# Kernel optimization log

Hardware: AMD Instinct MI355X
Metric: run time of the kernel (lower is better)

## Reference

```python
import jax, jax.numpy as jnp
import numpy as np

B, C, CE, DK, DV, H, W = 2, 64, 96, 64, 64, 96, 96
EPS = 1e-6


def setup_inputs() -> dict:
    key = jax.random.key(0)
    ks = jax.random.split(key, 8)
    s = lambda fan_in: 1.0 / np.sqrt(fan_in)
    return {
        "x": jax.random.normal(ks[0], (B, C, H, W), jnp.float32),
        "x_enc": jax.random.normal(ks[1], (B, CE, H, W), jnp.float32),
        "Wq": jax.random.uniform(ks[2], (DK, CE), jnp.float32, -s(CE), s(CE)),
        "bq": jax.random.uniform(ks[3], (DK,), jnp.float32, -s(CE), s(CE)),
        "Wk": jax.random.uniform(ks[4], (DK, CE), jnp.float32, -s(CE), s(CE)),
        "bk": jax.random.uniform(ks[5], (DK,), jnp.float32, -s(CE), s(CE)),
        "Wv": jax.random.uniform(ks[6], (DV, C), jnp.float32, -s(C), s(C)),
        "bv": jax.random.uniform(ks[7], (DV,), jnp.float32, -s(C), s(C)),
    }


def _l2norm(t):
    # F.normalize(dim=1): divide by channel-dim L2 norm, clamped at eps
    n = jnp.maximum(jnp.linalg.norm(t, axis=1, keepdims=True), EPS)
    return t / n


def reference(x, x_enc, Wq, bq, Wk, bk, Wv, bv):
    # 1x1 conv projections == pointwise channel GEMMs
    Q = jnp.einsum('oc,bchw->bohw', Wq, x_enc) + bq[None, :, None, None]
    K = jnp.einsum('oc,bchw->bohw', Wk, x_enc) + bk[None, :, None, None]
    V = jnp.einsum('oc,bchw->bohw', Wv, x) + bv[None, :, None, None]
    vshape = V.shape
    Q = _l2norm(Q.reshape(B, DK, H * W))  # [B, dk, L]
    K = _l2norm(K.reshape(B, DK, H * W))
    V = V.reshape(B, DV, H * W)           # [B, dv, L]
    # cosine-similarity attention over all spatial positions: A is [B, L, L]
    A = jax.nn.softmax(jnp.einsum('bqi,bqj->bij', Q, K), axis=-1)
    R = jnp.einsum('bij,bvj->bvi', A, V)   # [B, dv, L]
    return R.reshape(vshape)
```

## Files before the change

kernel.cpp:

```cpp
#include <hip/hip_runtime.h>

#define L_ 9216
#define TPS 9

typedef unsigned int uint;
typedef unsigned short ushort;
typedef __attribute__((ext_vector_type(8))) short short8;
typedef __attribute__((ext_vector_type(4))) float f32x4;
typedef __attribute__((ext_vector_type(16))) float f32x16;
typedef __attribute__((ext_vector_type(4))) unsigned uint4v;
typedef __attribute__((ext_vector_type(2))) unsigned uint2v;

#define MFMA32(a, b, c) __builtin_amdgcn_mfma_f32_32x32x16_bf16(a, b, c, 0, 0, 0)

#if __has_builtin(__builtin_amdgcn_exp2f)
#define EXP2(x) __builtin_amdgcn_exp2f(x)
#else
#define EXP2(x) exp2f(x)
#endif

#define GLOAD_LDS16(g, l)                                            \
  __builtin_amdgcn_global_load_lds(                                  \
      (const __attribute__((address_space(1))) unsigned int*)(g),    \
      (__attribute__((address_space(3))) unsigned int*)(l), 16, 0, 0)

union B8 {
  uint4v u;
  short8 s;
};

__device__ __forceinline__ ushort f2bf(float f) {
  uint u = __float_as_uint(f);
  return (ushort)((u + 0x7fffu + ((u >> 16) & 1u)) >> 16);
}

__device__ __forceinline__ f32x16 zero16() {
  f32x16 v;
#pragma unroll
  for (int i = 0; i < 16; i++) v[i] = 0.f;
  return v;
}

__global__ __launch_bounds__(256) void prep_kernel(
    const float* __restrict__ Wq, const float* __restrict__ Wk,
    const float* __restrict__ Wv, ushort* __restrict__ Wqb,
    ushort* __restrict__ Wkb, ushort* __restrict__ Wvb) {
  int i = blockIdx.x * 256 + threadIdx.x;
  if (i < 6144) {
    Wqb[i] = f2bf(Wq[i]);
    Wkb[i] = f2bf(Wk[i]);
  }
  if (i < 4096) Wvb[i] = f2bf(Wv[i]);
}

template <int CC, int TASK>
__device__ __forceinline__ void projm_body(
    const float* __restrict__ X,
    const ushort* __restrict__ Wb,
    const float* __restrict__ bias,
    ushort* __restrict__ dst) {
  constexpr int NKT = CC / 16;
  const int bx = blockIdx.x;
  const int b = bx / 288;
  const int p0 = (bx - b * 288) * 32;
  const int lane = threadIdx.x;
  const int ql = lane & 31;
  const int hs = lane >> 5;

  const float* Xb = X + (size_t)b * CC * L_ + p0 + ql;
  float xv[NKT * 8];
#pragma unroll
  for (int kt = 0; kt < NKT; kt++)
#pragma unroll
    for (int i = 0; i < 8; i++)
      xv[kt * 8 + i] = Xb[(size_t)(kt * 16 + hs * 8 + i) * L_];

  B8 bfr[NKT];
#pragma unroll
  for (int kt = 0; kt < NKT; kt++)
#pragma unroll
    for (int j = 0; j < 4; j++) {
      uint lo = f2bf(xv[kt * 8 + 2 * j]);
      uint hi = f2bf(xv[kt * 8 + 2 * j + 1]);
      bfr[kt].u[j] = lo | (hi << 16);
    }

  const ushort* Wr0 = Wb + (size_t)ql * CC + hs * 8;
  const ushort* Wr1 = Wb + (size_t)(32 + ql) * CC + hs * 8;

  f32x16 a0 = zero16(), a1 = zero16();
#pragma unroll
  for (int kt = 0; kt < NKT; kt++) {
    short8 w0 = *(const short8*)(Wr0 + kt * 16);
    short8 w1 = *(const short8*)(Wr1 + kt * 16);
    a0 = MFMA32(w0, bfr[kt].s, a0);
    a1 = MFMA32(w1, bfr[kt].s, a1);
  }

#pragma unroll
  for (int g = 0; g < 4; g++) {
    float4 b0 = *(const float4*)(bias + 8 * g + 4 * hs);
    float4 b1 = *(const float4*)(bias + 32 + 8 * g + 4 * hs);
    a0[4 * g + 0] += b0.x; a0[4 * g + 1] += b0.y;
    a0[4 * g + 2] += b0.z; a0[4 * g + 3] += b0.w;
    a1[4 * g + 0] += b1.x; a1[4 * g + 1] += b1.y;
    a1[4 * g + 2] += b1.z; a1[4 * g + 3] += b1.w;
  }

  if (TASK < 2) {
    float ss = 0.f;
#pragma unroll
    for (int r = 0; r < 16; r++) ss += a0[r] * a0[r] + a1[r] * a1[r];
    ss += __shfl_xor(ss, 32);
    float i0 = 1.0f / fmaxf(sqrtf(ss), 1e-6f);
    if (TASK == 0) i0 *= 1.44269504f;
    uint* d = (uint*)(dst + ((size_t)(b * L_ + p0 + ql)) * 64);
#pragma unroll
    for (int g = 0; g < 4; g++) {
      uint2v u0, u1;
      u0[0] = (uint)f2bf(a0[4 * g + 0] * i0) | ((uint)f2bf(a0[4 * g + 1] * i0) << 16);
      u0[1] = (uint)f2bf(a0[4 * g + 2] * i0) | ((uint)f2bf(a0[4 * g + 3] * i0) << 16);
      u1[0] = (uint)f2bf(a1[4 * g + 0] * i0) | ((uint)f2bf(a1[4 * g + 1] * i0) << 16);
      u1[1] = (uint)f2bf(a1[4 * g + 2] * i0) | ((uint)f2bf(a1[4 * g + 3] * i0) << 16);
      *(uint2v*)(d + 4 * g + 2 * hs) = u0;
      *(uint2v*)(d + 16 + 4 * g + 2 * hs) = u1;
    }
  } else {
#pragma unroll
    for (int r = 0; r < 16; r++) {
      int dv0 = (r & 3) + 8 * (r >> 2) + 4 * hs;
      dst[(size_t)(b * 64 + dv0) * L_ + p0 + ql] = f2bf(a0[r]);
      dst[(size_t)(b * 64 + 32 + dv0) * L_ + p0 + ql] = f2bf(a1[r]);
    }
  }
}

__global__ __launch_bounds__(64) void projm_kernel(
    const float* __restrict__ x, const float* __restrict__ x_enc,
    const ushort* __restrict__ Wqb, const float* __restrict__ bq,
    const ushort* __restrict__ Wkb, const float* __restrict__ bk,
    const ushort* __restrict__ Wvb, const float* __restrict__ bv,
    ushort* __restrict__ Qb, ushort* __restrict__ Kb,
    ushort* __restrict__ Vb) {
  const int task = blockIdx.y;
  if (task == 0)
    projm_body<96, 0>(x_enc, Wqb, bq, Qb);
  else if (task == 1)
    projm_body<96, 1>(x_enc, Wkb, bk, Kb);
  else
    projm_body<64, 2>(x, Wvb, bv, Vb);
}

__global__ __launch_bounds__(512) void attn_kernel(
    const ushort* __restrict__ Qb, const ushort* __restrict__ Kb,
    const ushort* __restrict__ Vb, ushort* __restrict__ OP,
    float* __restrict__ LB) {
  __shared__ __align__(16) ushort KV_l[4][2][4096];

  const int nwg = gridDim.x;
  const int chunk = nwg >> 3;
  const int bid = blockIdx.x;
  const int logical = (bid & 7) * chunk + (bid >> 3);
  const int split = logical / 72;
  const int qidx = logical - split * 72;
  const int b = qidx / 36;
  const int q0 = (qidx - b * 36) * 256;

  const int t = threadIdx.x;
  const int lane = t & 63;
  const int w = t >> 6;
  const int ql = lane & 31;
  const int hs = lane >> 5;

  const ushort* Kg = Kb + (size_t)b * L_ * 64;
  const ushort* Vg = Vb + (size_t)b * 64 * L_;

  const int qrow = q0 + w * 32 + ql;
  const ushort* Qr = Qb + ((size_t)(b * L_ + qrow)) * 64 + hs * 8;
  short8 qf[4];
  qf[0] = *(const short8*)(Qr);
  qf[1] = *(const short8*)(Qr + 16);
  qf[2] = *(const short8*)(Qr + 32);
  qf[3] = *(const short8*)(Qr + 48);

  B8 onesu;
  onesu.u[0] = 0x3F803F80u;
  onesu.u[1] = 0x3F803F80u;
  onesu.u[2] = 0x3F803F80u;
  onesu.u[3] = 0x3F803F80u;

  f32x16 o[2];
  o[0] = zero16();
  o[1] = zero16();
  f32x16 od = zero16();

  const int ksw = (ql & 7) << 3;
  const char* lds0 = (const char*)&KV_l[0][0][0];
  int arf[4];
#pragma unroll
  for (int m = 0; m < 4; m++)
    arf[m] = (ql * 64 + ((m * 16 + hs * 8) ^ ksw)) * 2;

  const int rr = t >> 3, pl = t & 7;
  const int psrc = (pl ^ (rr & 7)) << 3;
  const int j0base = split * TPS * 64;

#define STAGE(buf, j0)                                                     \
  {                                                                        \
    GLOAD_LDS16(Kg + (size_t)(j0)*64 + rr * 64 + psrc,                     \
                &KV_l[buf][0][w * 512]);                                   \
    GLOAD_LDS16(Vg + (size_t)rr * L_ + (j0) + psrc,                        \
                &KV_l[buf][1][w * 512]);                                   \
  }

#define QKMM(BUF, s0, s1)                                                  \
  {                                                                        \
    __builtin_amdgcn_s_setprio(1);                                         \
    _Pragma("unroll") for (int m = 0; m < 4; m++) {                        \
      short8 kf0 = *(const short8*)(lds0 + arf[m] + (BUF)*16384);          \
      short8 kf1 = *(const short8*)(lds0 + arf[m] + (BUF)*16384 + 4096);   \
      s0 = MFMA32(kf0, qf[m], s0);                                         \
      s1 = MFMA32(kf1, qf[m], s1);                                         \
    }                                                                      \
    __builtin_amdgcn_s_setprio(0);                                         \
  }

#define SMPK1(sa, pf, st)                                                  \
  {                                                                        \
    uint Wp[8];                                                            \
    _Pragma("unroll") for (int c = 0; c < 4; c++) _Pragma("unroll")        \
        for (int rp = 0; rp < 2; rp++) {                                   \
      int i0 = 4 * c + 2 * rp;                                             \
      float p0 = EXP2(sa[i0]);                                             \
      float p1 = EXP2(sa[i0 + 1]);                                         \
      Wp[2 * c + rp] = __builtin_amdgcn_perm(__float_as_uint(p1),          \
                                             __float_as_uint(p0),          \
                                             0x07060302u);                 \
    }                                                                      \
    _Pragma("unroll") for (int u = 0; u < 2; u++) {                        \
      auto ra = __builtin_amdgcn_permlane32_swap(Wp[4 * u + 0],            \
                                                 Wp[4 * u + 2], false,     \
                                                 false);                   \
      auto rb = __builtin_amdgcn_permlane32_swap(Wp[4 * u + 1],            \
                                                 Wp[4 * u + 3], false,     \
                                                 false);                   \
      uint4v fw;                                                           \
      fw[0] = ra[0];                                                       \
      fw[1] = rb[0];                                                       \
      fw[2] = ra[1];                                                       \
      fw[3] = rb[1];                                                       \
      pf[(st)*2 + u].u = fw;                                               \
    }                                                                      \
  }

#define PVDEN(BUF, pf)                                                     \
  {                                                                        \
    __builtin_amdgcn_s_setprio(1);                                         \
    _Pragma("unroll") for (int s = 0; s < 4; s++) od =                     \
        MFMA32(onesu.s, pf[s].s, od);                                      \
    _Pragma("unroll") for (int dt = 0; dt < 2; dt++) {                     \
      _Pragma("unroll") for (int s = 0; s < 4; s++) {                      \
        short8 vf = *(const short8*)(lds0 + arf[s] + (BUF)*16384 + 8192 +  \
                                     dt * 4096);                           \
        o[dt] = MFMA32(vf, pf[s].s, o[dt]);                                \
      }                                                                    \
    }                                                                      \
    __builtin_amdgcn_s_setprio(0);                                         \
  }

  B8 pfA[4], pfB[4];

  STAGE(0, j0base);
  STAGE(1, j0base + 64);
  STAGE(2, j0base + 128);
  asm volatile("s_waitcnt vmcnt(4)" ::: "memory");
  __builtin_amdgcn_s_barrier();
  {
    f32x16 s0 = zero16(), s1 = zero16();
    QKMM(0, s0, s1);
    SMPK1(s0, pfA, 0);
    SMPK1(s1, pfA, 1);
  }

#define PIPE_ITER(ib, pfCUR, pfNXT)                                        \
  {                                                                        \
    const int tt = t4 + (ib);                                              \
    if (tt + 2 < TPS) {                                                    \
      asm volatile("s_waitcnt vmcnt(2)" ::: "memory");                     \
    } else {                                                               \
      asm volatile("s_waitcnt vmcnt(0)" ::: "memory");                     \
    }                                                                      \
    __builtin_amdgcn_s_barrier();                                          \
    __builtin_amdgcn_sched_barrier(0);                                     \
    if (tt + 3 < TPS) STAGE(((ib) + 3) & 3, j0base + (tt + 3) * 64);       \
    f32x16 s0 = zero16(), s1 = zero16();                                   \
    QKMM((((ib) + 1) & 3), s0, s1);                                        \
    PVDEN(((ib)&3), pfCUR);                                                \
    SMPK1(s0, pfNXT, 0);                                                   \
    SMPK1(s1, pfNXT, 1);                                                   \
  }

  for (int t4 = 0; t4 < TPS - 1; t4 += 4) {
    PIPE_ITER(0, pfA, pfB)
    PIPE_ITER(1, pfB, pfA)
    PIPE_ITER(2, pfA, pfB)
    PIPE_ITER(3, pfB, pfA)
  }

  PVDEN(0, pfA);

  if (hs == 0) LB[(size_t)split * 2 * L_ + (size_t)b * L_ + qrow] = od[0];

  ushort* Ob = OP + (size_t)split * 2 * 64 * L_;
#pragma unroll
  for (int dt = 0; dt < 2; dt++)
#pragma unroll
    for (int r = 0; r < 16; r++) {
      int dv = dt * 32 + (r & 3) + 8 * (r >> 2) + 4 * hs;
      Ob[(size_t)(b * 64 + dv) * L_ + qrow] = f2bf(o[dt][r]);
    }
}

template <int NS>
__global__ __launch_bounds__(256) void combine_kernel(
    const ushort* __restrict__ OP, const float* __restrict__ LB,
    float* __restrict__ out) {
  const size_t e = ((size_t)blockIdx.x * 256 + threadIdx.x) * 8;
  const int bdv = (int)(e / L_);
  const int b = bdv >> 6;
  const int q = (int)(e % L_);
  float os[8], ls[8];
#pragma unroll
  for (int i = 0; i < 8; i++) { os[i] = 0.f; ls[i] = 0.f; }
#pragma unroll
  for (int s = 0; s < NS; s++) {
    uint4v pv = *(const uint4v*)(OP + (size_t)s * 2 * 64 * L_ + e);
    const float* lp = LB + (size_t)s * 2 * L_ + (size_t)b * L_ + q;
    f32x4 l0 = *(const f32x4*)(lp);
    f32x4 l1 = *(const f32x4*)(lp + 4);
#pragma unroll
    for (int i = 0; i < 4; i++) {
      os[2 * i] += __uint_as_float(pv[i] << 16);
      os[2 * i + 1] += __uint_as_float(pv[i] & 0xFFFF0000u);
      ls[i] += l0[i];
      ls[4 + i] += l1[i];
    }
  }
  float r[8];
#pragma unroll
  for (int i = 0; i < 8; i++) r[i] = os[i] / ls[i];
  *(f32x4*)(out + e) = *(const f32x4*)&r[0];
  *(f32x4*)(out + e + 4) = *(const f32x4*)&r[4];
}

extern "C" void kernel_launch(void* const* d_in, const int* in_sizes, int n_in,
                              void* d_out, int out_size, void* d_ws, size_t ws_size,
                              hipStream_t stream) {
  const float* x = (const float*)d_in[0];
  const float* x_enc = (const float*)d_in[1];
  const float* Wq = (const float*)d_in[2];
  const float* bq = (const float*)d_in[3];
  const float* Wk = (const float*)d_in[4];
  const float* bk = (const float*)d_in[5];
  const float* Wv = (const float*)d_in[6];
  const float* bv = (const float*)d_in[7];
  float* out = (float*)d_out;

  ushort* Qb = (ushort*)d_ws;
  ushort* Kb = Qb + (size_t)2 * L_ * 64;
  ushort* Vb = Kb + (size_t)2 * L_ * 64;
  ushort* Wqb = Vb + (size_t)2 * L_ * 64;
  ushort* Wkb = Wqb + 6144;
  ushort* Wvb = Wkb + 6144;
  const size_t qkv_bytes = (size_t)3 * 2 * L_ * 64 * 2 + 2 * (6144 + 6144 + 4096);

  const int SPLIT = 16;
  ushort* OP = (ushort*)((char*)d_ws + qkv_bytes);
  float* LB = (float*)(OP + (size_t)SPLIT * 2 * 64 * L_);

  prep_kernel<<<24, 256, 0, stream>>>(Wq, Wk, Wv, Wqb, Wkb, Wvb);
  projm_kernel<<<dim3(576, 3), 64, 0, stream>>>(x, x_enc, Wqb, bq, Wkb, bk,
                                                Wvb, bv, Qb, Kb, Vb);
  attn_kernel<<<72 * SPLIT, 512, 0, stream>>>(Qb, Kb, Vb, OP, LB);
  const int cgrid = (2 * 64 * L_ / 8) / 256;
  combine_kernel<16><<<cgrid, 256, 0, stream>>>(OP, LB, out);
}
```

Measured before the change: 86.91 us.

## Restructure attention loop into two-tile barrier intervals with per-tile softmax/PV

Replaces the software-pipelined loop, which overlapped the next tile's QK MFMAs with the current tile's PV, with a simpler schedule. Each interval waits for all loads, issues the next two stages, and processes two tiles fully. Within a tile, QK is followed by an exp/pack step and PV on half the fragments at a time, which drops the cross-iteration pf register state. It also adds launch_bounds occupancy hint 4 to cut register pressure and raise occupancy. In exchange it loses cross-tile MFMA overlap and uses fewer barriers but fully drains loads at each one.

```diff
diff --git a/kernel.cpp b/kernel.cpp
--- a/kernel.cpp
+++ b/kernel.cpp
@@ -151,7 +151,7 @@
     projm_body<64, 2>(x, Wvb, bv, Vb);
 }
 
-__global__ __launch_bounds__(512) void attn_kernel(
+__global__ __launch_bounds__(512, 4) void attn_kernel(
     const ushort* __restrict__ Qb, const ushort* __restrict__ Kb,
     const ushort* __restrict__ Vb, ushort* __restrict__ OP,
     float* __restrict__ LB) {
@@ -193,6 +193,7 @@
   o[0] = zero16();
   o[1] = zero16();
   f32x16 od = zero16();
+  f32x16 zv = zero16();
 
   const int ksw = (ql & 7) << 3;
   const char* lds0 = (const char*)&KV_l[0][0][0];
@@ -211,18 +212,6 @@
                 &KV_l[buf][0][w * 512]);                                   \
     GLOAD_LDS16(Vg + (size_t)rr * L_ + (j0) + psrc,                        \
                 &KV_l[buf][1][w * 512]);                                   \
-  }
-
-#define QKMM(BUF, s0, s1)                                                  \
-  {                                                                        \
-    __builtin_amdgcn_s_setprio(1);                                         \
-    _Pragma("unroll") for (int m = 0; m < 4; m++) {                        \
-      short8 kf0 = *(const short8*)(lds0 + arf[m] + (BUF)*16384);          \
-      short8 kf1 = *(const short8*)(lds0 + arf[m] + (BUF)*16384 + 4096);   \
-      s0 = MFMA32(kf0, qf[m], s0);                                         \
-      s1 = MFMA32(kf1, qf[m], s1);                                         \
-    }                                                                      \
-    __builtin_amdgcn_s_setprio(0);                                         \
   }
 
 #define SMPK1(sa, pf, st)                                                  \
@@ -253,61 +242,68 @@
     }                                                                      \
   }
 
-#define PVDEN(BUF, pf)                                                     \
+#define PVH(BUF, sA, sB)                                                   \
   {                                                                        \
     __builtin_amdgcn_s_setprio(1);                                         \
-    _Pragma("unroll") for (int s = 0; s < 4; s++) od =                     \
-        MFMA32(onesu.s, pf[s].s, od);                                      \
+    od = MFMA32(onesu.s, pf[sA].s, od);                                    \
+    od = MFMA32(onesu.s, pf[sB].s, od);                                    \
     _Pragma("unroll") for (int dt = 0; dt < 2; dt++) {                     \
-      _Pragma("unroll") for (int s = 0; s < 4; s++) {                      \
-        short8 vf = *(const short8*)(lds0 + arf[s] + (BUF)*16384 + 8192 +  \
-                                     dt * 4096);                           \
-        o[dt] = MFMA32(vf, pf[s].s, o[dt]);                                \
-      }                                                                    \
+      short8 vfa = *(const short8*)(lds0 + arf[sA] + (BUF)*16384 + 8192 +  \
+                                    dt * 4096);                            \
+      short8 vfb = *(const short8*)(lds0 + arf[sB] + (BUF)*16384 + 8192 +  \
+                                    dt * 4096);                            \
+      o[dt] = MFMA32(vfa, pf[sA].s, o[dt]);                                \
+      o[dt] = MFMA32(vfb, pf[sB].s, o[dt]);                                \
     }                                                                      \
     __builtin_amdgcn_s_setprio(0);                                         \
   }
 
-  B8 pfA[4], pfB[4];
+#define TILE(BUF)                                                          \
+  {                                                                        \
+    f32x16 s0, s1;                                                         \
+    __builtin_amdgcn_s_setprio(1);                                         \
+    {                                                                      \
+      short8 kf0 = *(const short8*)(lds0 + arf[0] + (BUF)*16384);          \
+      short8 kf1 = *(const short8*)(lds0 + arf[0] + (BUF)*16384 + 4096);   \
+      s0 = MFMA32(kf0, qf[0], zv);                                         \
+      s1 = MFMA32(kf1, qf[0], zv);                                         \
+    }                                                                      \
+    _Pragma("unroll") for (int m = 1; m < 4; m++) {                        \
+      short8 kf0 = *(const short8*)(lds0 + arf[m] + (BUF)*16384);          \
+      short8 kf1 = *(const short8*)(lds0 + arf[m] + (BUF)*16384 + 4096);   \
+      s0 = MFMA32(kf0, qf[m], s0);                                         \
+      s1 = MFMA32(kf1, qf[m], s1);                                         \
+    }                                                                      \
+    __builtin_amdgcn_s_setprio(0);                                         \
+    B8 pf[4];                                                              \
+    SMPK1(s0, pf, 0);                                                      \
+    PVH(BUF, 0, 1);                                                        \
+    SMPK1(s1, pf, 1);                                                      \
+    PVH(BUF, 2, 3);                                                        \
+  }
+
+#define INTERVAL(bA, bB, tS0, tS1, nst)                                    \
+  {                                                                        \
+    asm volatile("s_waitcnt vmcnt(0)" ::: "memory");                       \
+    __builtin_amdgcn_s_barrier();                                          \
+    __builtin_amdgcn_sched_barrier(0);                                     \
+    if ((nst) >= 1) STAGE((tS0) & 3, j0base + (tS0)*64);                   \
+    if ((nst) >= 2) STAGE((tS1) & 3, j0base + (tS1)*64);                   \
+    TILE(bA);                                                              \
+    TILE(bB);                                                              \
+  }
 
   STAGE(0, j0base);
   STAGE(1, j0base + 64);
-  STAGE(2, j0base + 128);
-  asm volatile("s_waitcnt vmcnt(4)" ::: "memory");
+
+  INTERVAL(0, 1, 2, 3, 2)
+  INTERVAL(2, 3, 4, 5, 2)
+  INTERVAL(0, 1, 6, 7, 2)
+  INTERVAL(2, 3, 8, 9, 1)
+
+  asm volatile("s_waitcnt vmcnt(0)" ::: "memory");
   __builtin_amdgcn_s_barrier();
-  {
-    f32x16 s0 = zero16(), s1 = zero16();
-    QKMM(0, s0, s1);
-    SMPK1(s0, pfA, 0);
-    SMPK1(s1, pfA, 1);
-  }
-
-#define PIPE_ITER(ib, pfCUR, pfNXT)                                        \
-  {                                                                        \
-    const int tt = t4 + (ib);                                              \
-    if (tt + 2 < TPS) {                                                    \
-      asm volatile("s_waitcnt vmcnt(2)" ::: "memory");                     \
-    } else {                                                               \
-      asm volatile("s_waitcnt vmcnt(0)" ::: "memory");                     \
-    }                                                                      \
-    __builtin_amdgcn_s_barrier();                                          \
-    __builtin_amdgcn_sched_barrier(0);                                     \
-    if (tt + 3 < TPS) STAGE(((ib) + 3) & 3, j0base + (tt + 3) * 64);       \
-    f32x16 s0 = zero16(), s1 = zero16();                                   \
-    QKMM((((ib) + 1) & 3), s0, s1);                                        \
-    PVDEN(((ib)&3), pfCUR);                                                \
-    SMPK1(s0, pfNXT, 0);                                                   \
-    SMPK1(s1, pfNXT, 1);                                                   \
-  }
-
-  for (int t4 = 0; t4 < TPS - 1; t4 += 4) {
-    PIPE_ITER(0, pfA, pfB)
-    PIPE_ITER(1, pfB, pfA)
-    PIPE_ITER(2, pfA, pfB)
-    PIPE_ITER(3, pfB, pfA)
-  }
-
-  PVDEN(0, pfA);
+  TILE(0);
 
   if (hs == 0) LB[(size_t)split * 2 * L_ + (size_t)b * L_ + qrow] = od[0];
 
```

Result: slower. 97.60 us (+12.3%).
